# Performance work log

Hardware: AMD Instinct MI355X
Metric: run time of the kernel (lower is better)

## Reference

```python
import jax, jax.numpy as jnp
import numpy as np

IN_FEATURES = 4096
OUT_FEATURES = 16384
TOKENS = 32


def setup_inputs() -> dict:
    key = jax.random.key(0)
    k1, k2, k3, k4 = jax.random.split(key, 4)
    x = jax.random.normal(k1, (TOKENS, IN_FEATURES), dtype=jnp.float16)
    # int8-valued weights in [-127, 127]
    weight_int8 = jax.random.randint(k2, (OUT_FEATURES, IN_FEATURES), -127, 128, dtype=jnp.int32)
    # per-output-channel scale, positive (amax/127 in the original)
    scale = (jax.random.uniform(k3, (OUT_FEATURES,), dtype=jnp.float32) * 0.02 + 1e-4).astype(jnp.float16)
    bias = jax.random.normal(k4, (OUT_FEATURES,), dtype=jnp.float16)
    return {"x": x, "weight_int8": weight_int8, "scale": scale, "bias": bias}


def reference(x, weight_int8, scale, bias):
    # Dequantize int8 weights to compute dtype with per-row scale, then linear.
    w = weight_int8.astype(jnp.float16) * scale[:, None]          # [out, in] fp16
    return jnp.dot(x, w.T) + bias                                  # [tokens, out]
```

## Files before the change

### kernel.cpp

```cpp
#include <hip/hip_runtime.h>
#include <hip/hip_bf16.h>


typedef __attribute__((ext_vector_type(4))) int    i32x4;
typedef __attribute__((ext_vector_type(4))) float  f32x4;
typedef __attribute__((ext_vector_type(8))) short  s16x8;
typedef __attribute__((ext_vector_type(8))) __bf16 bf16x8;

constexpr int K = 4096;
constexpr int N = 16384;
constexpr int T = 32;
constexpr int KSPLIT = 2;
constexpr int KPW = K / KSPLIT;
constexpr int BK = 256;
constexpr int NT = KPW / BK;
constexpr int ROWPITCH = 1024 + 16;
constexpr size_t XB_OFF = 0;
constexpr size_t PART_OFF = 262144;

__device__ inline unsigned short f2bf_rne(float f) {
    unsigned u = __builtin_bit_cast(unsigned, f);
    u += 0x7FFF + ((u >> 16) & 1);
    return (unsigned short)(u >> 16);
}

__device__ inline bf16x8 cvtW(i32x4 lo, i32x4 hi) {
    s16x8 r;
#pragma unroll
    for (int i = 0; i < 4; ++i) {
        r[i]     = (short)(__builtin_bit_cast(unsigned, (float)lo[i]) >> 16);
        r[i + 4] = (short)(__builtin_bit_cast(unsigned, (float)hi[i]) >> 16);
    }
    return __builtin_bit_cast(bf16x8, r);
}

__global__ __launch_bounds__(256) void xcvt_kernel(const float* __restrict__ x,
                                                   unsigned short* __restrict__ xb) {
    const int i = (blockIdx.x * 256 + threadIdx.x) * 8;
    f32x4 lo = *reinterpret_cast<const f32x4*>(x + i);
    f32x4 hi = *reinterpret_cast<const f32x4*>(x + i + 4);
    s16x8 r;
#pragma unroll
    for (int j = 0; j < 4; ++j) {
        r[j]     = (short)f2bf_rne(lo[j]);
        r[j + 4] = (short)f2bf_rne(hi[j]);
    }
    *reinterpret_cast<s16x8*>(xb + i) = r;
}

__global__ __launch_bounds__(256, 2) void w8gemm_kernel(
    const __bf16* __restrict__ xb,
    const int* __restrict__ w,
    float* __restrict__ partial)
{
    extern __shared__ char smem[];

    const int lane = threadIdx.x & 63;
    const int wave = threadIdx.x >> 6;
    const int n16  = lane & 15;
    const int quad = lane >> 4;

    const int g  = blockIdx.x & 255;
    const int ks = blockIdx.x >> 8;
    const int kbase = ks * KPW;

    const char* gW0 = (const char*)w
        + ((size_t)(g * 64 + wave * 16) * K + kbase) * 4 + (size_t)lane * 16;
    char* lds0 = smem + (wave * 16) * ROWPITCH + lane * 16;

    auto stage = [&](int it) {
        const char* gp = gW0 + (size_t)it * BK * 4;
#pragma unroll
        for (int j = 0; j < 16; ++j) {
            __builtin_amdgcn_global_load_lds(
                (const __attribute__((address_space(1))) void*)(gp + (size_t)j * K * 4),
                (__attribute__((address_space(3))) void*)(lds0 + j * ROWPITCH),
                16, 0, 0);
        }
    };

    const __bf16* __restrict__ xr0 = xb + (size_t)n16 * K + kbase + quad * 8;
    const __bf16* __restrict__ xr1 = xr0 + (size_t)16 * K;

    f32x4 acc0 = {0.f, 0.f, 0.f, 0.f};
    f32x4 acc1 = {0.f, 0.f, 0.f, 0.f};

    const char* lrow = smem + (wave * 16 + n16) * ROWPITCH + quad * 32;

    stage(0);
#pragma unroll 1
    for (int it = 0; it < NT; ++it) {
        bf16x8 aX0[8], aX1[8];
#pragma unroll
        for (int s = 0; s < 8; ++s) {
            const int off = it * BK + s * 32;
            aX0[s] = *reinterpret_cast<const bf16x8*>(xr0 + off);
            aX1[s] = *reinterpret_cast<const bf16x8*>(xr1 + off);
        }
        __syncthreads();
#pragma unroll
        for (int s = 0; s < 8; ++s) {
            i32x4 b0 = *reinterpret_cast<const i32x4*>(lrow + s * 128);
            i32x4 b1 = *reinterpret_cast<const i32x4*>(lrow + s * 128 + 16);
            bf16x8 bf = cvtW(b0, b1);
            acc0 = __builtin_amdgcn_mfma_f32_16x16x32_bf16(aX0[s], bf, acc0, 0, 0, 0);
            acc1 = __builtin_amdgcn_mfma_f32_16x16x32_bf16(aX1[s], bf, acc1, 0, 0, 0);
        }
        __syncthreads();
        if (it + 1 < NT) stage(it + 1);
    }

    const int c = g * 64 + wave * 16 + n16;
    float* __restrict__ p = partial + (size_t)ks * T * N;
#pragma unroll
    for (int v = 0; v < 4; ++v) {
        const int row = quad * 4 + v;
        p[(size_t)row * N + c]        = acc0[v];
        p[(size_t)(row + 16) * N + c] = acc1[v];
    }
}

__global__ __launch_bounds__(256) void reduce_kernel(
    const float* __restrict__ partial,
    const float* __restrict__ scale,
    const float* __restrict__ bias,
    float* __restrict__ out)
{
    const int i = (blockIdx.x * 256 + threadIdx.x) * 4;
    const int c = i & (N - 1);
    f32x4 s = *reinterpret_cast<const f32x4*>(partial + i);
#pragma unroll
    for (int ks = 1; ks < KSPLIT; ++ks) {
        f32x4 pv = *reinterpret_cast<const f32x4*>(partial + (size_t)ks * T * N + i);
        s[0] += pv[0]; s[1] += pv[1]; s[2] += pv[2]; s[3] += pv[3];
    }
    f32x4 sc = *reinterpret_cast<const f32x4*>(scale + c);
    f32x4 bi = *reinterpret_cast<const f32x4*>(bias + c);
    f32x4 r = {s[0] * sc[0] + bi[0], s[1] * sc[1] + bi[1],
               s[2] * sc[2] + bi[2], s[3] * sc[3] + bi[3]};
    *reinterpret_cast<f32x4*>(out + i) = r;
}

extern "C" void kernel_launch(void* const* d_in, const int* in_sizes, int n_in,
                              void* d_out, int out_size, void* d_ws, size_t ws_size,
                              hipStream_t stream) {
    const float* x     = (const float*)d_in[0];
    const int*   w     = (const int*)d_in[1];
    const float* scale = (const float*)d_in[2];
    const float* bias  = (const float*)d_in[3];
    float* out = (float*)d_out;

    unsigned short* xb = (unsigned short*)((char*)d_ws + XB_OFF);
    float* part        = (float*)((char*)d_ws + PART_OFF);

    xcvt_kernel<<<dim3(64), dim3(256), 0, stream>>>(x, xb);
    w8gemm_kernel<<<dim3(256 * KSPLIT), dim3(256), 64 * ROWPITCH, stream>>>(
        (const __bf16*)xb, w, part);
    reduce_kernel<<<dim3((T * N / 4) / 256), dim3(256), 0, stream>>>(
        part, scale, bias, out);
}
```

Before: 383.2 us.

## Replace cross-block split-K with intra-block wave split-K and fused epilogue

Each block now owns 16 output columns, and its four waves split the K dimension among themselves. Partial sums are reduced through shared memory, with scale and bias applied in the same kernel. This removes the global partial buffer and the separate reduce launch, and raises the block count to 1024 with smaller per-block LDS. The cost is an LDS reduction with extra barriers, plus uncoalesced scalar output stores of 16 columns per token row.

```diff
diff --git a/kernel.cpp b/kernel.cpp
--- a/kernel.cpp
+++ b/kernel.cpp
@@ -9,14 +9,10 @@
 
 constexpr int K = 4096;
 constexpr int N = 16384;
-constexpr int T = 32;
-constexpr int KSPLIT = 2;
-constexpr int KPW = K / KSPLIT;
-constexpr int BK = 256;
-constexpr int NT = KPW / BK;
-constexpr int ROWPITCH = 1024 + 16;
+constexpr int BKI = 1024;
+constexpr int NT = K / BKI;
+constexpr int PITCH = 4096 + 16;
 constexpr size_t XB_OFF = 0;
-constexpr size_t PART_OFF = 262144;
 
 __device__ inline unsigned short f2bf_rne(float f) {
     unsigned u = __builtin_bit_cast(unsigned, f);
@@ -51,94 +47,89 @@
 __global__ __launch_bounds__(256, 2) void w8gemm_kernel(
     const __bf16* __restrict__ xb,
     const int* __restrict__ w,
-    float* __restrict__ partial)
+    const float* __restrict__ scale,
+    const float* __restrict__ bias,
+    float* __restrict__ out)
 {
     extern __shared__ char smem[];
 
-    const int lane = threadIdx.x & 63;
-    const int wave = threadIdx.x >> 6;
+    const int tid  = threadIdx.x;
+    const int lane = tid & 63;
+    const int wave = tid >> 6;
     const int n16  = lane & 15;
     const int quad = lane >> 4;
 
-    const int g  = blockIdx.x & 255;
-    const int ks = blockIdx.x >> 8;
-    const int kbase = ks * KPW;
-
-    const char* gW0 = (const char*)w
-        + ((size_t)(g * 64 + wave * 16) * K + kbase) * 4 + (size_t)lane * 16;
-    char* lds0 = smem + (wave * 16) * ROWPITCH + lane * 16;
+    const int c0 = blockIdx.x * 16;
 
     auto stage = [&](int it) {
-        const char* gp = gW0 + (size_t)it * BK * 4;
 #pragma unroll
-        for (int j = 0; j < 16; ++j) {
-            __builtin_amdgcn_global_load_lds(
-                (const __attribute__((address_space(1))) void*)(gp + (size_t)j * K * 4),
-                (__attribute__((address_space(3))) void*)(lds0 + j * ROWPITCH),
-                16, 0, 0);
+        for (int j = 0; j < 4; ++j) {
+            const int row = wave * 4 + j;
+            const char* gsrc = (const char*)(w + (size_t)(c0 + row) * K + it * BKI)
+                               + (size_t)lane * 16;
+            char* ldst = smem + row * PITCH + lane * 16;
+#pragma unroll
+            for (int s = 0; s < 4; ++s) {
+                __builtin_amdgcn_global_load_lds(
+                    (const __attribute__((address_space(1))) void*)(gsrc + s * 1024),
+                    (__attribute__((address_space(3))) void*)(ldst + s * 1024),
+                    16, 0, 0);
+            }
         }
     };
 
-    const __bf16* __restrict__ xr0 = xb + (size_t)n16 * K + kbase + quad * 8;
+    const char* lrow = smem + n16 * PITCH + quad * 32 + wave * 1024;
+    const __bf16* __restrict__ xr0 = xb + (size_t)n16 * K + wave * 256 + quad * 8;
     const __bf16* __restrict__ xr1 = xr0 + (size_t)16 * K;
 
     f32x4 acc0 = {0.f, 0.f, 0.f, 0.f};
     f32x4 acc1 = {0.f, 0.f, 0.f, 0.f};
-
-    const char* lrow = smem + (wave * 16 + n16) * ROWPITCH + quad * 32;
 
     stage(0);
 #pragma unroll 1
     for (int it = 0; it < NT; ++it) {
         bf16x8 aX0[8], aX1[8];
 #pragma unroll
-        for (int s = 0; s < 8; ++s) {
-            const int off = it * BK + s * 32;
-            aX0[s] = *reinterpret_cast<const bf16x8*>(xr0 + off);
-            aX1[s] = *reinterpret_cast<const bf16x8*>(xr1 + off);
+        for (int j = 0; j < 8; ++j) {
+            const int off = it * BKI + j * 32;
+            aX0[j] = *reinterpret_cast<const bf16x8*>(xr0 + off);
+            aX1[j] = *reinterpret_cast<const bf16x8*>(xr1 + off);
         }
         __syncthreads();
 #pragma unroll
-        for (int s = 0; s < 8; ++s) {
-            i32x4 b0 = *reinterpret_cast<const i32x4*>(lrow + s * 128);
-            i32x4 b1 = *reinterpret_cast<const i32x4*>(lrow + s * 128 + 16);
+        for (int j = 0; j < 8; ++j) {
+            i32x4 b0 = *reinterpret_cast<const i32x4*>(lrow + j * 128);
+            i32x4 b1 = *reinterpret_cast<const i32x4*>(lrow + j * 128 + 16);
             bf16x8 bf = cvtW(b0, b1);
-            acc0 = __builtin_amdgcn_mfma_f32_16x16x32_bf16(aX0[s], bf, acc0, 0, 0, 0);
-            acc1 = __builtin_amdgcn_mfma_f32_16x16x32_bf16(aX1[s], bf, acc1, 0, 0, 0);
+            acc0 = __builtin_amdgcn_mfma_f32_16x16x32_bf16(aX0[j], bf, acc0, 0, 0, 0);
+            acc1 = __builtin_amdgcn_mfma_f32_16x16x32_bf16(aX1[j], bf, acc1, 0, 0, 0);
         }
         __syncthreads();
         if (it + 1 < NT) stage(it + 1);
     }
 
-    const int c = g * 64 + wave * 16 + n16;
-    float* __restrict__ p = partial + (size_t)ks * T * N;
+    __syncthreads();
+    float* red = (float*)smem;
 #pragma unroll
     for (int v = 0; v < 4; ++v) {
-        const int row = quad * 4 + v;
-        p[(size_t)row * N + c]        = acc0[v];
-        p[(size_t)(row + 16) * N + c] = acc1[v];
+        red[wave * 512 + lane * 8 + v]     = acc0[v];
+        red[wave * 512 + lane * 8 + 4 + v] = acc1[v];
     }
-}
-
-__global__ __launch_bounds__(256) void reduce_kernel(
-    const float* __restrict__ partial,
-    const float* __restrict__ scale,
-    const float* __restrict__ bias,
-    float* __restrict__ out)
-{
-    const int i = (blockIdx.x * 256 + threadIdx.x) * 4;
-    const int c = i & (N - 1);
-    f32x4 s = *reinterpret_cast<const f32x4*>(partial + i);
+    __syncthreads();
 #pragma unroll
-    for (int ks = 1; ks < KSPLIT; ++ks) {
-        f32x4 pv = *reinterpret_cast<const f32x4*>(partial + (size_t)ks * T * N + i);
-        s[0] += pv[0]; s[1] += pv[1]; s[2] += pv[2]; s[3] += pv[3];
+    for (int pp = 0; pp < 2; ++pp) {
+        const int p = tid + pp * 256;
+        float s = red[p] + red[512 + p] + red[1024 + p] + red[1536 + p];
+        const int pl   = p >> 3;
+        const int r    = p & 7;
+        const int half = r >> 2;
+        const int v    = r & 3;
+        const int pn   = pl & 15;
+        const int pq   = pl >> 4;
+        const int token = half * 16 + pq * 4 + v;
+        const int c = c0 + pn;
+        out[(size_t)token * N + c] = s * scale[c] + bias[c];
     }
-    f32x4 sc = *reinterpret_cast<const f32x4*>(scale + c);
-    f32x4 bi = *reinterpret_cast<const f32x4*>(bias + c);
-    f32x4 r = {s[0] * sc[0] + bi[0], s[1] * sc[1] + bi[1],
-               s[2] * sc[2] + bi[2], s[3] * sc[3] + bi[3]};
-    *reinterpret_cast<f32x4*>(out + i) = r;
 }
 
 extern "C" void kernel_launch(void* const* d_in, const int* in_sizes, int n_in,
@@ -151,11 +142,8 @@
     float* out = (float*)d_out;
 
     unsigned short* xb = (unsigned short*)((char*)d_ws + XB_OFF);
-    float* part        = (float*)((char*)d_ws + PART_OFF);
 
     xcvt_kernel<<<dim3(64), dim3(256), 0, stream>>>(x, xb);
-    w8gemm_kernel<<<dim3(256 * KSPLIT), dim3(256), 64 * ROWPITCH, stream>>>(
-        (const __bf16*)xb, w, part);
-    reduce_kernel<<<dim3((T * N / 4) / 256), dim3(256), 0, stream>>>(
-        part, scale, bias, out);
+    w8gemm_kernel<<<dim3(N / 16), dim3(256), 16 * PITCH, stream>>>(
+        (const __bf16*)xb, w, scale, bias, out);
 }
```

New measurement: 369.4 us. 1.04x faster.
